# Optimization experiments

Measured on AMD Instinct MI355X. Metric: run time of the kernel, lower is better.

## Reference

```python
import jax, jax.numpy as jnp
import numpy as np

N = 50000        # total nodes
E = 600000       # total edges (before self loops)
NID = 16         # node_input_dim
D = 128          # hidden_dim
H = 4            # heads
C = D // H       # out_channels per head = 32
L = 4            # num_layers
EPS = 1e-5
NEG_SLOPE = 0.2


def setup_inputs() -> dict:
    key = jax.random.key(0)
    ks = jax.random.split(key, 16)
    s = 0.05
    return {
        "node_types": jax.random.randint(ks[0], (N,), 0, 3),
        "edge_index": jax.random.randint(ks[1], (2, E), 0, N),
        # embedding + input projection (Linear -> LayerNorm -> ReLU)
        "emb_table": jax.random.normal(ks[2], (3, NID), jnp.float32) * s,
        "proj_W": jax.random.normal(ks[3], (NID, D), jnp.float32) * s,
        "proj_b": jnp.zeros((D,), jnp.float32),
        "proj_g": jnp.ones((D,), jnp.float32),
        "proj_beta": jnp.zeros((D,), jnp.float32),
        # per-layer GATv2 params (stacked over L layers)
        "Wl": jax.random.normal(ks[4], (L, D, D), jnp.float32) * s,   # lin_l weight
        "bl": jnp.zeros((L, D), jnp.float32),                          # lin_l bias
        "Wr": jax.random.normal(ks[5], (L, D, D), jnp.float32) * s,   # lin_r weight
        "br": jnp.zeros((L, D), jnp.float32),                          # lin_r bias
        "att": jax.random.normal(ks[6], (L, H, C), jnp.float32) * s,  # attention vector
        "gat_bias": jnp.zeros((L, D), jnp.float32),                   # output bias (concat)
        # per-layer LayerNorm
        "ln_g": jnp.ones((L, D), jnp.float32),
        "ln_b": jnp.zeros((L, D), jnp.float32),
    }


def layer_norm(x, g, b):
    mu = jnp.mean(x, axis=-1, keepdims=True)
    var = jnp.mean(jnp.square(x - mu), axis=-1, keepdims=True)
    return (x - mu) * jax.lax.rsqrt(var + EPS) * g + b


def gatv2_layer(x, src, dst, Wl, bl, Wr, br, att, bias):
    # x: [N, D]; src/dst: [E+N] (self loops included)
    n = x.shape[0]
    xl = (x @ Wl + bl).reshape(n, H, C)   # source transform
    xr = (x @ Wr + br).reshape(n, H, C)   # destination transform
    e = jax.nn.leaky_relu(xl[src] + xr[dst], NEG_SLOPE)          # [E', H, C]
    logits = jnp.einsum('ehc,hc->eh', e, att)                    # [E', H]
    m = jax.ops.segment_max(logits, dst, num_segments=n)         # segment softmax (stable)
    alpha = jnp.exp(logits - m[dst])
    denom = jax.ops.segment_sum(alpha, dst, num_segments=n)
    alpha = alpha / denom[dst]                                   # [E', H]
    msg = xl[src] * alpha[:, :, None]                            # [E', H, C]
    out = jax.ops.segment_sum(msg, dst, num_segments=n)          # [N, H, C]
    return out.reshape(n, H * C) + bias


def reference(node_types, edge_index, emb_table, proj_W, proj_b, proj_g, proj_beta,
              Wl, bl, Wr, br, att, gat_bias, ln_g, ln_b):
    n = node_types.shape[0]
    loop = jnp.arange(n, dtype=edge_index.dtype)
    src = jnp.concatenate([edge_index[0], loop])   # add self loops
    dst = jnp.concatenate([edge_index[1], loop])

    x = emb_table[node_types]                      # [N, NID]
    x = jax.nn.relu(layer_norm(x @ proj_W + proj_b, proj_g, proj_beta))  # input_proj (dropout=id at eval)

    for i in range(L):
        x_res = x
        x = gatv2_layer(x, src, dst, Wl[i], bl[i], Wr[i], br[i], att[i], gat_bias[i])
        x = layer_norm(x + x_res, ln_g[i], ln_b[i])
        x = jax.nn.relu(x)
    return x
```

## Files before the change

kernel.cpp:

```cpp
#include <hip/hip_runtime.h>
#include <hip/hip_bf16.h>
#include <math.h>

#define D      128
#define NID    16
#define H      4
#define CH     32
#define NLAYER 4
#define EPS    1e-5f
#define NEG    0.2f
#define LOG2E  1.442695040888963f
#define CNTMASK 1023

typedef __attribute__((ext_vector_type(8))) short short8;
typedef __attribute__((ext_vector_type(4))) float floatx4;
typedef _Float16 h2 __attribute__((ext_vector_type(2)));
typedef float fx2 __attribute__((ext_vector_type(2)));

__device__ __forceinline__ float2 bf2_to_f2(unsigned int u) {
    float2 r;
    unsigned int lo = u << 16;
    unsigned int hi = u & 0xffff0000u;
    r.x = __uint_as_float(lo);
    r.y = __uint_as_float(hi);
    return r;
}

__device__ __forceinline__ unsigned short f2bf(float f) {
    __hip_bfloat16 h = __float2bfloat16(f);
    return *reinterpret_cast<unsigned short*>(&h);
}

__device__ __forceinline__ unsigned short f2h(float f) {
    _Float16 h = (_Float16)f;
    unsigned short u;
    __builtin_memcpy(&u, &h, 2);
    return u;
}

__device__ __forceinline__ h2 u2h2(unsigned int u) {
    h2 v;
    __builtin_memcpy(&v, &u, 4);
    return v;
}

__device__ __forceinline__ h2 pkrtz(float a, float b) {
    auto r = __builtin_amdgcn_cvt_pkrtz(a, b);
    h2 out;
    __builtin_memcpy(&out, &r, 4);
    return out;
}

__device__ __forceinline__ unsigned char f2fp8(float v) {
    int pk = __builtin_amdgcn_cvt_pk_fp8_f32(v, v, 0, false);
    return (unsigned char)(pk & 0xff);
}

__device__ __forceinline__ void fp8x4_to_h2x2(unsigned int w, h2* out) {
    fx2 f0 = __builtin_amdgcn_cvt_pk_f32_fp8((int)w, false);
    fx2 f1 = __builtin_amdgcn_cvt_pk_f32_fp8((int)w, true);
    out[0] = pkrtz(f0[0], f0[1]);
    out[1] = pkrtz(f1[0], f1[1]);
}


__global__ __launch_bounds__(256) void scan_blocks_kernel(const int* __restrict__ deg, int* __restrict__ offs,
                                                          int* __restrict__ bsum, int n) {
    __shared__ int sw[8];
    int t = threadIdx.x;
    int i = blockIdx.x * 256 + t;
    int v = 0;
    if (i < n) {
        int d = deg[i];
        v = (d & CNTMASK) + ((d >> 10) & CNTMASK) + ((d >> 20) & CNTMASK) + 1;
    }
    int lane = t & 63, w = t >> 6;
    int x = v;
    #pragma unroll
    for (int off = 1; off < 64; off <<= 1) {
        int y = __shfl_up(x, off, 64);
        if (lane >= off) x += y;
    }
    if (lane == 63) sw[w] = x;
    __syncthreads();
    if (t == 0) {
        int s = 0;
        for (int k = 0; k < 4; ++k) { int tv = sw[k]; sw[k] = s; s += tv; }
        sw[4] = s;
    }
    __syncthreads();
    int excl = x - v + sw[w];
    if (i < n) offs[i] = excl;
    if (t == 255) bsum[blockIdx.x] = sw[4];
}

__global__ __launch_bounds__(256) void scan_add_kernel(int* __restrict__ offs, const int* __restrict__ bsum,
                                                       int* __restrict__ cursor, int n, int nb, int total) {
    __shared__ int sw[8];
    __shared__ int sS;
    int t = threadIdx.x;
    int bid = blockIdx.x;
    int v = (t < bid && t < nb) ? bsum[t] : 0;
    int lane = t & 63, w = t >> 6;
    #pragma unroll
    for (int off = 32; off > 0; off >>= 1) v += __shfl_xor(v, off, 64);
    if (lane == 0) sw[w] = v;
    __syncthreads();
    if (t == 0) sS = sw[0] + sw[1] + sw[2] + sw[3];
    __syncthreads();
    int S = sS;
    int i = bid * 256 + t;
    if (i < n) {
        int o = offs[i] + S;
        offs[i] = o;
        cursor[i] = o;
    }
    if (i == 0) offs[n] = total;
}

__global__ __launch_bounds__(256) void setup_kernel(
    const float* __restrict__ emb,
    const float* __restrict__ W, const float* __restrict__ pb,
    const float* __restrict__ pg, const float* __restrict__ pbeta,
    const float* __restrict__ Wl, const float* __restrict__ Wr,
    const float* __restrict__ bl, const float* __restrict__ br,
    const float* __restrict__ att,
    unsigned short* __restrict__ wt,
    const int* __restrict__ srcs, const int* __restrict__ dsts,
    const int* __restrict__ types, int* __restrict__ deg, int e,
    unsigned short* __restrict__ x3bf, float* __restrict__ xl3f,
    float* __restrict__ w9,
    int nbE) {
    __shared__ float sbuf[2048];
    __shared__ float semb[3 * NID];
    int blk = blockIdx.x;
    int t = threadIdx.x;
    if (blk < 512) {
        int idx = blk * 256 + t;
        int k    = idx & (D - 1);
        int nrow = (idx >> 7) & (D - 1);
        int s    = (idx >> 14) & 1;
        int l    = idx >> 15;
        const float* Wm = s ? Wr : Wl;
        wt[idx] = f2bf(Wm[(size_t)l * D * D + (size_t)k * D + nrow]);
    } else if (blk < 512 + nbE) {
        int i = (blk - 512) * 256 + t;
        if (i < e) {
            int ty = types[srcs[i]];
            atomicAdd(&deg[dsts[i]], 1 << (10 * ty));
        }
    } else {
        float* p3  = sbuf;
        float* x3s = sbuf + 384;
        float* red = sbuf + 768;
        float* xlf = sbuf + 772;
        float* xrf = sbuf + 1156;
        for (int i = t; i < 3 * NID; i += 256) semb[i] = emb[i];
        __syncthreads();
        int c = t;
        if (c < D) {
            float wcol[NID];
            #pragma unroll
            for (int k = 0; k < NID; ++k) wcol[k] = W[k * D + c];
            float bc = pb[c];
            #pragma unroll
            for (int ty = 0; ty < 3; ++ty) {
                float a = bc;
                #pragma unroll
                for (int k = 0; k < NID; ++k) a = fmaf(semb[ty * NID + k], wcol[k], a);
                p3[ty * D + c] = a;
            }
        }
        __syncthreads();
        #pragma unroll 1
        for (int ty = 0; ty < 3; ++ty) {
            float v = (c < D) ? p3[ty * D + c] : 0.0f;
            float s = v, sq = v * v;
            #pragma unroll
            for (int off = 1; off < 64; off <<= 1) {
                s  += __shfl_xor(s, off, 64);
                sq += __shfl_xor(sq, off, 64);
            }
            if ((t & 63) == 0 && t < 128) { red[(t >> 6) * 2] = s; red[(t >> 6) * 2 + 1] = sq; }
            __syncthreads();
            float S = red[0] + red[2], SQ = red[1] + red[3];
            float mu = S * (1.0f / D), var = SQ * (1.0f / D) - mu * mu;
            float r = rsqrtf(var + EPS);
            if (c < D) {
                float o = fmaxf((p3[ty * D + c] - mu) * r * pg[c] + pbeta[c], 0.0f);
                unsigned short bfv = f2bf(o);
                x3s[ty * D + c] = __uint_as_float((unsigned int)bfv << 16);
                x3bf[ty * D + c] = bfv;
            }
            __syncthreads();
        }
        if (c < D) {
            #pragma unroll 1
            for (int ty = 0; ty < 3; ++ty) {
                float al = bl[c], ar = br[c];
                for (int k = 0; k < D; ++k) {
                    float xv = x3s[ty * D + k];
                    al = fmaf(xv, Wl[(size_t)k * D + c], al);
                    ar = fmaf(xv, Wr[(size_t)k * D + c], ar);
                }
                xlf[ty * D + c] = al;
                xrf[ty * D + c] = ar;
                xl3f[ty * D + c] = al;
            }
        }
        __syncthreads();
        if (c < D) {
            float av = att[c];
            int h = c >> 5;
            #pragma unroll 1
            for (int tyd = 0; tyd < 3; ++tyd) {
                #pragma unroll 1
                for (int tys = 0; tys < 3; ++tys) {
                    float ev = xlf[tys * D + c] + xrf[tyd * D + c];
                    ev = fmaxf(ev, NEG * ev);
                    float p = av * ev;
                    #pragma unroll
                    for (int off = 1; off < 32; off <<= 1) p += __shfl_xor(p, off, 32);
                    if ((c & 31) == 0) w9[(tyd * 3 + tys) * H + h] = exp2f(p * LOG2E);
                }
            }
        }
    }
}

__global__ __launch_bounds__(256) void gat_l0_dense_kernel(
    const int* __restrict__ deg, const int* __restrict__ types,
    const float* __restrict__ w9, const float* __restrict__ xl3f,
    const unsigned short* __restrict__ x3bf,
    const float* __restrict__ gbias,
    const float* __restrict__ lng, const float* __restrict__ lnb,
    unsigned short* __restrict__ xout, int n, int ngrp) {
    int t = threadIdx.x;
    int lane = t & 63, w = t >> 6;
    int c0 = 2 * lane;
    int h = c0 >> 5;
    for (int grp = blockIdx.x; grp < ngrp; grp += gridDim.x) {
        int node = grp * 4 + w;
        if (node >= n) continue;
        int tyn = types[node];
        int d = deg[node];
        float cnt[3];
        cnt[0] = (float)(d & CNTMASK);
        cnt[1] = (float)((d >> 10) & CNTMASK);
        cnt[2] = (float)((d >> 20) & CNTMASK);
        cnt[tyn] += 1.0f;
        float cw0 = cnt[0] * w9[(tyn * 3 + 0) * H + h];
        float cw1 = cnt[1] * w9[(tyn * 3 + 1) * H + h];
        float cw2 = cnt[2] * w9[(tyn * 3 + 2) * H + h];
        float inv = 1.0f / (cw0 + cw1 + cw2);
        float n0 = cw0 * xl3f[0 * D + c0] + cw1 * xl3f[1 * D + c0] + cw2 * xl3f[2 * D + c0];
        float n1 = cw0 * xl3f[0 * D + c0 + 1] + cw1 * xl3f[1 * D + c0 + 1] + cw2 * xl3f[2 * D + c0 + 1];
        float2 xi = bf2_to_f2(*(const unsigned int*)(x3bf + (size_t)tyn * D + c0));
        float v0 = fmaf(n0, inv, gbias[c0]     + xi.x);
        float v1 = fmaf(n1, inv, gbias[c0 + 1] + xi.y);
        float s = v0 + v1, sq = v0 * v0 + v1 * v1;
        #pragma unroll
        for (int off = 1; off < 64; off <<= 1) {
            s  += __shfl_xor(s, off, 64);
            sq += __shfl_xor(sq, off, 64);
        }
        float mu  = s * (1.0f / D);
        float var = sq * (1.0f / D) - mu * mu;
        float r   = rsqrtf(var + EPS);
        v0 = fmaxf((v0 - mu) * r * lng[c0]     + lnb[c0],     0.0f);
        v1 = fmaxf((v1 - mu) * r * lng[c0 + 1] + lnb[c0 + 1], 0.0f);
        unsigned int packed = (unsigned int)f2bf(v0) | ((unsigned int)f2bf(v1) << 16);
        *(unsigned int*)(xout + (size_t)node * D + c0) = packed;
    }
}

__global__ __launch_bounds__(256) void dual_gemm_mfma_kernel(
    const unsigned short* __restrict__ x, const unsigned short* __restrict__ wt,
    const float* __restrict__ bl, const float* __restrict__ br,
    unsigned char* __restrict__ xl, unsigned short* __restrict__ xr, int n,
    int ntiles,
    const int* __restrict__ srcs, const int* __restrict__ dsts, int e,
    int* __restrict__ cursor, int* __restrict__ csr_src) {
    __shared__ __align__(16) unsigned short sa[64 * 136];
    int t = threadIdx.x;
    if (blockIdx.x >= ntiles) {
        int i = (blockIdx.x - ntiles) * 256 + t;
        if (i < e) {
            int pos = atomicAdd(&cursor[dsts[i]], 1);
            csr_src[pos] = srcs[i];
        } else if (i < e + n) {
            int node = i - e;
            int pos = atomicAdd(&cursor[node], 1);
            csr_src[pos] = node;
        }
        return;
    }
    int nbase = blockIdx.x * 64;
    int rows = n - nbase; if (rows > 64) rows = 64;
    int lane = t & 63, w = t >> 6;
    int L = lane & 15, q = lane >> 4;
    int s  = w >> 1;
    int n0 = (w & 1) * 64;
    const unsigned short* wb = wt + ((size_t)s * D + n0) * D;
    short8 b[4][4];
    #pragma unroll
    for (int kk = 0; kk < 4; ++kk)
        #pragma unroll
        for (int ni = 0; ni < 4; ++ni)
            b[kk][ni] = *(const short8*)(wb + (size_t)(ni * 16 + L) * D + kk * 32 + q * 8);
    {
        int r   = t >> 2;
        int seg = t & 3;
        uint4* drow = (uint4*)(sa + r * 136 + seg * 32);
        if (r < rows) {
            const uint4* srow = (const uint4*)(x + (size_t)(nbase + r) * D + seg * 32);
            drow[0] = srow[0]; drow[1] = srow[1]; drow[2] = srow[2]; drow[3] = srow[3];
        } else {
            uint4 z = make_uint4(0, 0, 0, 0);
            drow[0] = z; drow[1] = z; drow[2] = z; drow[3] = z;
        }
    }
    __syncthreads();
    floatx4 acc[4][4];
    #pragma unroll
    for (int mi = 0; mi < 4; ++mi)
        #pragma unroll
        for (int ni = 0; ni < 4; ++ni)
            acc[mi][ni] = (floatx4){0.0f, 0.0f, 0.0f, 0.0f};
    #pragma unroll
    for (int kk = 0; kk < 4; ++kk) {
        int ko = kk * 32 + q * 8;
        short8 a[4];
        #pragma unroll
        for (int mi = 0; mi < 4; ++mi)
            a[mi] = *(const short8*)(sa + (mi * 16 + L) * 136 + ko);
        #pragma unroll
        for (int mi = 0; mi < 4; ++mi)
            #pragma unroll
            for (int ni = 0; ni < 4; ++ni)
                acc[mi][ni] = __builtin_amdgcn_mfma_f32_16x16x32_bf16(a[mi], b[kk][ni], acc[mi][ni], 0, 0, 0);
    }
    const float* bias = s ? br : bl;
    __syncthreads();
    if (s == 0) {
        unsigned char* sb = (unsigned char*)sa;
        #pragma unroll
        for (int ni = 0; ni < 4; ++ni) {
            int col = n0 + ni * 16 + L;
            float bv = bias[col];
            #pragma unroll
            for (int mi = 0; mi < 4; ++mi) {
                #pragma unroll
                for (int r = 0; r < 4; ++r) {
                    int row = mi * 16 + q * 4 + r;
                    sb[row * 272 + col] = f2fp8(acc[mi][ni][r] + bv);
                }
            }
        }
    }
    __syncthreads();
    {
        unsigned char* sb = (unsigned char*)sa;
        #pragma unroll
        for (int c = 0; c < 2; ++c) {
            int chunk = c * 256 + t;
            int row   = chunk >> 3;
            int off   = (chunk & 7) * 16;
            if (row < rows) {
                uint4 v = *(const uint4*)(sb + row * 272 + off);
                *(uint4*)(xl + (size_t)(nbase + row) * D + off) = v;
            }
        }
    }
    __syncthreads();
    if (s == 1) {
        #pragma unroll
        for (int ni = 0; ni < 4; ++ni) {
            int col = n0 + ni * 16 + L;
            float bv = bias[col];
            #pragma unroll
            for (int mi = 0; mi < 4; ++mi) {
                #pragma unroll
                for (int r = 0; r < 4; ++r) {
                    int row = mi * 16 + q * 4 + r;
                    sa[row * 136 + col] = f2h(acc[mi][ni][r] + bv);
                }
            }
        }
    }
    __syncthreads();
    #pragma unroll
    for (int c = 0; c < 4; ++c) {
        int chunk = c * 256 + t;
        int row   = chunk >> 4;
        int off   = (chunk & 15) * 8;
        if (row < rows) {
            short8 v = *(const short8*)(sa + row * 136 + off);
            *(short8*)(xr + (size_t)(nbase + row) * D + off) = v;
        }
    }
}

__global__ __launch_bounds__(256) void gat_agg_kernel(
    const unsigned char* __restrict__ xl, const unsigned short* __restrict__ xr,
    const unsigned short* __restrict__ xin,
    const int* __restrict__ offs, const int* __restrict__ csr_src,
    const float* __restrict__ att,
    const float* __restrict__ gbias,
    const float* __restrict__ lng, const float* __restrict__ lnb,
    unsigned short* __restrict__ xout_bf, float* __restrict__ xout_f32, int n) {
    int t = threadIdx.x;
    int lane = t & 63, w = t >> 6;
    int node = blockIdx.x * 4 + w;
    if (node >= n) return;
    int g  = lane >> 4;
    int l  = lane & 15;
    int cb = l * 8;
    h2 xr2[4], at2[4];
    {
        uint4 u = *(const uint4*)(xr + (size_t)node * D + cb);
        xr2[0] = u2h2(u.x); xr2[1] = u2h2(u.y); xr2[2] = u2h2(u.z); xr2[3] = u2h2(u.w);
        float4 t0 = *(const float4*)(att + cb);
        float4 t1 = *(const float4*)(att + cb + 4);
        at2[0] = (h2){(_Float16)(t0.x * LOG2E), (_Float16)(t0.y * LOG2E)};
        at2[1] = (h2){(_Float16)(t0.z * LOG2E), (_Float16)(t0.w * LOG2E)};
        at2[2] = (h2){(_Float16)(t1.x * LOG2E), (_Float16)(t1.y * LOG2E)};
        at2[3] = (h2){(_Float16)(t1.z * LOG2E), (_Float16)(t1.w * LOG2E)};
    }
    h2 acch[4];
    #pragma unroll
    for (int i = 0; i < 4; ++i) acch[i] = (h2){(_Float16)0.0f, (_Float16)0.0f};
    float lsum = 0.0f;
    int s0 = offs[node], s1 = offs[node + 1];
    int j0 = s0 + g;
    bool val_c = j0 < s1;
    int src_c = csr_src[val_c ? j0 : s0];
    uint2 u_c = *(const uint2*)(xl + (size_t)src_c * D + cb);
    int j1 = j0 + 4;
    bool val_n = j1 < s1;
    int src_n = csr_src[val_n ? j1 : s0];
    uint2 u_n = *(const uint2*)(xl + (size_t)src_n * D + cb);
    int j2 = j0 + 8;
    bool val_2 = j2 < s1;
    int src_2 = csr_src[val_2 ? j2 : s0];
    for (int j = s0; j < s1; j += 4) {
        uint2 u_2 = *(const uint2*)(xl + (size_t)src_2 * D + cb);
        int j3 = j + 12 + g;
        bool val_3 = j3 < s1;
        int src_3 = csr_src[val_3 ? j3 : s0];
        h2 xv2[4];
        fp8x4_to_h2x2(u_c.x, xv2);
        fp8x4_to_h2x2(u_c.y, xv2 + 2);
        float p = 0.0f;
        #pragma unroll
        for (int i = 0; i < 4; ++i) {
            h2 e  = xv2[i] + xr2[i];
            h2 el = __builtin_elementwise_max(e, e * (_Float16)NEG);
            p = __builtin_amdgcn_fdot2(el, at2[i], p, false);
        }
        p += __shfl_xor(p, 1, 64);
        p += __shfl_xor(p, 2, 64);
        float wgt = val_c ? exp2f(p) : 0.0f;
        lsum += wgt;
        _Float16 wh = (_Float16)wgt;
        h2 w2 = {wh, wh};
        #pragma unroll
        for (int i = 0; i < 4; ++i) acch[i] += w2 * xv2[i];
        u_c = u_n; u_n = u_2;
        val_c = val_n; val_n = val_2;
        val_2 = val_3; src_2 = src_3;
    }
    float acc[8];
    #pragma unroll
    for (int i = 0; i < 4; ++i) {
        acc[2 * i]     = (float)acch[i][0];
        acc[2 * i + 1] = (float)acch[i][1];
    }
    #pragma unroll
    for (int i = 0; i < 8; ++i) {
        acc[i] += __shfl_xor(acc[i], 16, 64);
        acc[i] += __shfl_xor(acc[i], 32, 64);
    }
    lsum += __shfl_xor(lsum, 16, 64);
    lsum += __shfl_xor(lsum, 32, 64);
    float inv = 1.0f / lsum;
    float xi[8];
    {
        uint4 u = *(const uint4*)(xin + (size_t)node * D + cb);
        float2 a = bf2_to_f2(u.x), b = bf2_to_f2(u.y), c = bf2_to_f2(u.z), d = bf2_to_f2(u.w);
        xi[0]=a.x; xi[1]=a.y; xi[2]=b.x; xi[3]=b.y; xi[4]=c.x; xi[5]=c.y; xi[6]=d.x; xi[7]=d.y;
    }
    float4 gb0 = *(const float4*)(gbias + cb);
    float4 gb1 = *(const float4*)(gbias + cb + 4);
    float gb[8] = {gb0.x, gb0.y, gb0.z, gb0.w, gb1.x, gb1.y, gb1.z, gb1.w};
    float v[8];
    #pragma unroll
    for (int i = 0; i < 8; ++i) v[i] = fmaf(acc[i], inv, gb[i] + xi[i]);
    float s = 0.0f, sq = 0.0f;
    #pragma unroll
    for (int i = 0; i < 8; ++i) { s += v[i]; sq = fmaf(v[i], v[i], sq); }
    #pragma unroll
    for (int off = 1; off < 16; off <<= 1) {
        s  += __shfl_xor(s, off, 64);
        sq += __shfl_xor(sq, off, 64);
    }
    float mu  = s * (1.0f / D);
    float var = sq * (1.0f / D) - mu * mu;
    float r   = rsqrtf(var + EPS);
    float4 lg0 = *(const float4*)(lng + cb);
    float4 lg1 = *(const float4*)(lng + cb + 4);
    float4 lb0 = *(const float4*)(lnb + cb);
    float4 lb1 = *(const float4*)(lnb + cb + 4);
    float lg[8] = {lg0.x, lg0.y, lg0.z, lg0.w, lg1.x, lg1.y, lg1.z, lg1.w};
    float lb[8] = {lb0.x, lb0.y, lb0.z, lb0.w, lb1.x, lb1.y, lb1.z, lb1.w};
    float o[8];
    #pragma unroll
    for (int i = 0; i < 8; ++i) o[i] = fmaxf((v[i] - mu) * r * lg[i] + lb[i], 0.0f);
    if (g == 0) {
        if (xout_f32) {
            *(float4*)(xout_f32 + (size_t)node * D + cb)     = make_float4(o[0], o[1], o[2], o[3]);
            *(float4*)(xout_f32 + (size_t)node * D + cb + 4) = make_float4(o[4], o[5], o[6], o[7]);
        } else {
            unsigned int p0 = (unsigned int)f2bf(o[0]) | ((unsigned int)f2bf(o[1]) << 16);
            unsigned int p1 = (unsigned int)f2bf(o[2]) | ((unsigned int)f2bf(o[3]) << 16);
            unsigned int p2 = (unsigned int)f2bf(o[4]) | ((unsigned int)f2bf(o[5]) << 16);
            unsigned int p3 = (unsigned int)f2bf(o[6]) | ((unsigned int)f2bf(o[7]) << 16);
            *(uint4*)(xout_bf + (size_t)node * D + cb) = make_uint4(p0, p1, p2, p3);
        }
    }
}

extern "C" void kernel_launch(void* const* d_in, const int* in_sizes, int n_in,
                              void* d_out, int out_size, void* d_ws, size_t ws_size,
                              hipStream_t stream) {
    const int*   node_types = (const int*)d_in[0];
    const int*   edge_index = (const int*)d_in[1];
    const float* emb        = (const float*)d_in[2];
    const float* projW      = (const float*)d_in[3];
    const float* projb      = (const float*)d_in[4];
    const float* projg      = (const float*)d_in[5];
    const float* projbeta   = (const float*)d_in[6];
    const float* Wl         = (const float*)d_in[7];
    const float* bl         = (const float*)d_in[8];
    const float* Wr         = (const float*)d_in[9];
    const float* br         = (const float*)d_in[10];
    const float* att        = (const float*)d_in[11];
    const float* gbias      = (const float*)d_in[12];
    const float* lng        = (const float*)d_in[13];
    const float* lnb        = (const float*)d_in[14];
    float* out = (float*)d_out;

    int n = in_sizes[0];
    int e = in_sizes[1] / 2;
    const int* srcs = edge_index;
    const int* dsts = edge_index + e;

    char* p = (char*)d_ws;
    auto carve = [&](size_t bytes) {
        char* q = p;
        p += (bytes + 255) & ~(size_t)255;
        return q;
    };
    int*   deg     = (int*)carve((size_t)n * 4);
    int*   offs    = (int*)carve((size_t)(n + 1) * 4);
    int*   cursor  = (int*)carve((size_t)n * 4);
    int*   bsum    = (int*)carve(256 * 4);
    int*   csr_src = (int*)carve((size_t)(e + n) * 4);
    unsigned short* xbuf = (unsigned short*)carve((size_t)n * D * 2);
    unsigned char*  xlb  = (unsigned char*)carve((size_t)n * D);
    unsigned short* xrb  = (unsigned short*)carve((size_t)n * D * 2);
    unsigned short* wt   = (unsigned short*)carve((size_t)NLAYER * 2 * D * D * 2);
    unsigned short* x3bf = (unsigned short*)carve(3 * D * 2);
    float*          xl3f = (float*)carve(3 * D * 4);
    float*          w9   = (float*)carve(9 * H * 4);

    int nb = (n + 255) / 256;
    int nbE = (e + 255) / 256;
    int ntiles = (n + 63) / 64;
    int nscat  = (e + n + 255) / 256;
    int ngrp   = (n + 3) / 4;

    hipMemsetAsync(deg, 0, (size_t)n * 4, stream);

    setup_kernel<<<512 + nbE + 1, 256, 0, stream>>>(
        emb, projW, projb, projg, projbeta,
        Wl, Wr, bl, br, att, wt, srcs, dsts, node_types, deg, e,
        x3bf, xl3f, w9, nbE);

    scan_blocks_kernel<<<nb, 256, 0, stream>>>(deg, offs, bsum, n);
    scan_add_kernel<<<nb, 256, 0, stream>>>(offs, bsum, cursor, n, nb, e + n);

    gat_l0_dense_kernel<<<2048, 256, 0, stream>>>(
        deg, node_types, w9, xl3f, x3bf,
        gbias, lng, lnb, xbuf, n, ngrp);

    for (int layer = 1; layer < NLAYER; ++layer) {
        int extra = (layer == 1) ? nscat : 0;
        dual_gemm_mfma_kernel<<<ntiles + extra, 256, 0, stream>>>(
            xbuf, wt + (size_t)layer * 2 * D * D,
            bl + (size_t)layer * D, br + (size_t)layer * D, xlb, xrb, n,
            ntiles, srcs, dsts, e, cursor, csr_src);
        bool last = (layer == NLAYER - 1);
        gat_agg_kernel<<<ngrp, 256, 0, stream>>>(
            xlb, xrb, xbuf, offs, csr_src,
            att + (size_t)layer * H * CH, gbias + (size_t)layer * D,
            lng + (size_t)layer * D, lnb + (size_t)layer * D,
            last ? (unsigned short*)nullptr : xbuf, last ? out : (float*)nullptr, n);
    }
}
```

Measured before the change: 328.1 us.

## Bucket edges by destination range before CSR scatter for locality

The degree-count pass now also partitions edges into 128 destination-range buckets (512 nodes each) in a global staging buffer, using per-block shared-memory histograms and one global atomic per bucket. The CSR scatter then runs one block per bucket, so the cursor atomics and csr_src writes of each block hit a narrow, cache-resident address range instead of random locations across the whole array. Edges that overflow a bucket's fixed capacity go to an overflow list that a single block processes. This adds an extra write and read of all edge pairs plus a memset, and leaves the scatter with only about 130 blocks, so parallelism may be limited.

```diff
diff --git a/kernel.cpp b/kernel.cpp
--- a/kernel.cpp
+++ b/kernel.cpp
@@ -11,6 +11,8 @@
 #define NEG    0.2f
 #define LOG2E  1.442695040888963f
 #define CNTMASK 1023
+#define NBUCK  128
+#define BCAP   8192
 
 typedef __attribute__((ext_vector_type(8))) short short8;
 typedef __attribute__((ext_vector_type(4))) float floatx4;
@@ -128,9 +130,11 @@
     unsigned short* __restrict__ wt,
     const int* __restrict__ srcs, const int* __restrict__ dsts,
     const int* __restrict__ types, int* __restrict__ deg, int e,
+    int* __restrict__ bcur, int* __restrict__ gbuck,
+    int* __restrict__ ovfcnt, int* __restrict__ govf,
     unsigned short* __restrict__ x3bf, float* __restrict__ xl3f,
     float* __restrict__ w9,
-    int nbE) {
+    int nbP1) {
     __shared__ float sbuf[2048];
     __shared__ float semb[3 * NID];
     int blk = blockIdx.x;
@@ -143,11 +147,44 @@
         int l    = idx >> 15;
         const float* Wm = s ? Wr : Wl;
         wt[idx] = f2bf(Wm[(size_t)l * D * D + (size_t)k * D + nrow]);
-    } else if (blk < 512 + nbE) {
-        int i = (blk - 512) * 256 + t;
-        if (i < e) {
-            int ty = types[srcs[i]];
-            atomicAdd(&deg[dsts[i]], 1 << (10 * ty));
+    } else if (blk < 512 + nbP1) {
+        int* hcnt  = (int*)sbuf;
+        int* hbase = hcnt + NBUCK;
+        int* hloc  = hbase + NBUCK;
+        if (t < NBUCK) { hcnt[t] = 0; hloc[t] = 0; }
+        __syncthreads();
+        int ebase = (blk - 512) * 2048;
+        int my_src[8], my_dst[8], my_b[8];
+        #pragma unroll
+        for (int k = 0; k < 8; ++k) {
+            int i = ebase + k * 256 + t;
+            my_b[k] = -1;
+            if (i < e) {
+                int s = srcs[i], d = dsts[i];
+                my_src[k] = s; my_dst[k] = d;
+                int b = d >> 9;
+                my_b[k] = b;
+                atomicAdd(&hcnt[b], 1);
+                int ty = types[s];
+                atomicAdd(&deg[d], 1 << (10 * ty));
+            }
+        }
+        __syncthreads();
+        if (t < NBUCK) hbase[t] = atomicAdd(&bcur[t], hcnt[t]);
+        __syncthreads();
+        #pragma unroll
+        for (int k = 0; k < 8; ++k) {
+            int b = my_b[k];
+            if (b >= 0) {
+                int off = atomicAdd(&hloc[b], 1);
+                int pos = hbase[b] + off;
+                if (pos < BCAP) {
+                    *(int2*)&gbuck[((size_t)b * BCAP + pos) * 2] = make_int2(my_src[k], my_dst[k]);
+                } else {
+                    int op = atomicAdd(ovfcnt, 1);
+                    *(int2*)&govf[(size_t)op * 2] = make_int2(my_src[k], my_dst[k]);
+                }
+            }
         }
     } else {
         float* p3  = sbuf;
@@ -278,20 +315,35 @@
     const unsigned short* __restrict__ x, const unsigned short* __restrict__ wt,
     const float* __restrict__ bl, const float* __restrict__ br,
     unsigned char* __restrict__ xl, unsigned short* __restrict__ xr, int n,
-    int ntiles,
-    const int* __restrict__ srcs, const int* __restrict__ dsts, int e,
+    int ntiles, int nself,
+    const int* __restrict__ bcur, const int* __restrict__ gbuck,
+    const int* __restrict__ ovfcnt, const int* __restrict__ govf,
     int* __restrict__ cursor, int* __restrict__ csr_src) {
     __shared__ __align__(16) unsigned short sa[64 * 136];
     int t = threadIdx.x;
     if (blockIdx.x >= ntiles) {
-        int i = (blockIdx.x - ntiles) * 256 + t;
-        if (i < e) {
-            int pos = atomicAdd(&cursor[dsts[i]], 1);
-            csr_src[pos] = srcs[i];
-        } else if (i < e + n) {
-            int node = i - e;
-            int pos = atomicAdd(&cursor[node], 1);
-            csr_src[pos] = node;
+        int xb = blockIdx.x - ntiles;
+        if (xb < NBUCK) {
+            int cnt = bcur[xb]; if (cnt > BCAP) cnt = BCAP;
+            const int* bp = gbuck + (size_t)xb * BCAP * 2;
+            for (int i = t; i < cnt; i += 256) {
+                int s = bp[2 * i], d = bp[2 * i + 1];
+                int pos = atomicAdd(&cursor[d], 1);
+                csr_src[pos] = s;
+            }
+        } else if (xb < NBUCK + nself) {
+            int node = (xb - NBUCK) * 256 + t;
+            if (node < n) {
+                int pos = atomicAdd(&cursor[node], 1);
+                csr_src[pos] = node;
+            }
+        } else {
+            int cnt = *ovfcnt;
+            for (int i = t; i < cnt; i += 256) {
+                int s = govf[2 * i], d = govf[2 * i + 1];
+                int pos = atomicAdd(&cursor[d], 1);
+                csr_src[pos] = s;
+            }
         }
         return;
     }
@@ -573,19 +625,26 @@
     unsigned short* x3bf = (unsigned short*)carve(3 * D * 2);
     float*          xl3f = (float*)carve(3 * D * 4);
     float*          w9   = (float*)carve(9 * H * 4);
+    int*   bstate  = (int*)carve(256 * 4);
+    int*   bcur    = bstate;
+    int*   ovfcnt  = bstate + 128;
+    int*   gbuck   = (int*)carve((size_t)NBUCK * BCAP * 8);
+    int*   govf    = (int*)carve((size_t)e * 8);
 
     int nb = (n + 255) / 256;
-    int nbE = (e + 255) / 256;
+    int nbP1 = (e + 2047) / 2048;
     int ntiles = (n + 63) / 64;
-    int nscat  = (e + n + 255) / 256;
+    int nself = (n + 255) / 256;
     int ngrp   = (n + 3) / 4;
 
     hipMemsetAsync(deg, 0, (size_t)n * 4, stream);
-
-    setup_kernel<<<512 + nbE + 1, 256, 0, stream>>>(
+    hipMemsetAsync(bstate, 0, 256 * 4, stream);
+
+    setup_kernel<<<512 + nbP1 + 1, 256, 0, stream>>>(
         emb, projW, projb, projg, projbeta,
         Wl, Wr, bl, br, att, wt, srcs, dsts, node_types, deg, e,
-        x3bf, xl3f, w9, nbE);
+        bcur, gbuck, ovfcnt, govf,
+        x3bf, xl3f, w9, nbP1);
 
     scan_blocks_kernel<<<nb, 256, 0, stream>>>(deg, offs, bsum, n);
     scan_add_kernel<<<nb, 256, 0, stream>>>(offs, bsum, cursor, n, nb, e + n);
@@ -595,11 +654,11 @@
         gbias, lng, lnb, xbuf, n, ngrp);
 
     for (int layer = 1; layer < NLAYER; ++layer) {
-        int extra = (layer == 1) ? nscat : 0;
+        int extra = (layer == 1) ? (NBUCK + nself + 1) : 0;
         dual_gemm_mfma_kernel<<<ntiles + extra, 256, 0, stream>>>(
             xbuf, wt + (size_t)layer * 2 * D * D,
             bl + (size_t)layer * D, br + (size_t)layer * D, xlb, xrb, n,
-            ntiles, srcs, dsts, e, cursor, csr_src);
+            ntiles, nself, bcur, gbuck, ovfcnt, govf, cursor, csr_src);
         bool last = (layer == NLAYER - 1);
         gat_agg_kernel<<<ngrp, 256, 0, stream>>>(
             xlb, xrb, xbuf, offs, csr_src,
```

Result: no change. 327.8 us (-0.1%).
